# Kernel tuning notes

Measured on AMD Instinct MI355X. Metric: run time of the kernel, lower is better.

The kernel has to match this reference:

```python
import jax, jax.numpy as jnp
import numpy as np

NODELEN = 10


def setup_inputs() -> dict:
    key = jax.random.key(0)
    ks = jax.random.split(key, 16)
    N, DEG = 200000, 32
    IN, H1, H2, EMB = 2 * NODELEN, 15, 10, 5
    features = jax.random.normal(ks[0], (N, NODELEN), dtype=jnp.float32)
    adj = jax.random.randint(ks[1], (N, DEG), 0, N, dtype=jnp.int32)
    s = 0.1
    inp = {
        'features': features,
        'adj': adj,
        'We1': jax.random.normal(ks[2], (H1, IN), dtype=jnp.float32) * s,
        'be1': jnp.zeros((H1,), dtype=jnp.float32),
        'We2': jax.random.normal(ks[3], (H2, H1), dtype=jnp.float32) * s,
        'be2': jnp.zeros((H2,), dtype=jnp.float32),
        'We3': jax.random.normal(ks[4], (EMB, H2), dtype=jnp.float32) * s,
        'be3': jnp.zeros((EMB,), dtype=jnp.float32),
        'Wd1': jax.random.normal(ks[5], (H2, EMB), dtype=jnp.float32) * s,
        'bd1': jnp.zeros((H2,), dtype=jnp.float32),
        'Wd2': jax.random.normal(ks[6], (H1, H2), dtype=jnp.float32) * s,
        'bd2': jnp.zeros((H1,), dtype=jnp.float32),
        'Wd3': jax.random.normal(ks[7], (IN, H1), dtype=jnp.float32) * s,
        'bd3': jnp.zeros((IN,), dtype=jnp.float32),
    }
    return inp


def _autoencoder(x, We1, be1, We2, be2, We3, be3, Wd1, bd1, Wd2, bd2, Wd3, bd3):
    # torch nn.Linear: y = x @ W.T + b ; dropout is identity in eval
    h = jax.nn.relu(x @ We1.T + be1)
    h = jax.nn.relu(h @ We2.T + be2)
    encoded = h @ We3.T + be3
    h = jax.nn.relu(encoded @ Wd1.T + bd1)
    h = jax.nn.relu(h @ Wd2.T + bd2)
    decoded = h @ Wd3.T + bd3
    return encoded, decoded


def reference(features, adj, We1, be1, We2, be2, We3, be3,
              Wd1, bd1, Wd2, bd2, Wd3, bd3):
    # depth-2 recursive neighbor aggregation (aggregate_neighbors):
    # hop 1: mean of raw neighbor features, element 0 zeroed
    h1 = jnp.mean(features[adj], axis=1)          # [N, deg, F] -> [N, F]
    h1 = h1.at[:, 0].set(0.0)
    # hop 2: mean of hop-1 features of neighbors, element 0 zeroed
    agg = jnp.mean(h1[adj], axis=1)
    agg = agg.at[:, 0].set(0.0)
    # generate_embedding: concat(self, aggregated), zero positions 0 and NODELEN
    emb = jnp.concatenate([features, agg], axis=1)
    emb = emb.at[:, 0].set(0.0).at[:, NODELEN].set(0.0)
    encoded, decoded = _autoencoder(emb, We1, be1, We2, be2, We3, be3,
                                    Wd1, bd1, Wd2, bd2, Wd3, bd3)
    return encoded, decoded, emb
```

## Files before the change

kernel.cpp:

```cpp
#include <hip/hip_runtime.h>

#define NODELEN 10
#define DEG 32
#define NPB 64


#if defined(__has_builtin)
#if __has_builtin(__builtin_amdgcn_cvt_pk_f32_fp8)
#define USE_HW_FP8_DECODE 1
#endif
#endif

typedef float floatx2 __attribute__((ext_vector_type(2)));

__device__ __forceinline__ float fp8_to_f32_sw(unsigned b) {
    unsigned s = (b & 0x80u) << 24;
    unsigned e = (b >> 3) & 0xFu;
    unsigned m = b & 0x7u;
    float fn = __uint_as_float(s | ((e + 120u) << 23) | (m << 20));
    float fs = __uint_as_float(s | __float_as_uint((float)m * 0.001953125f));
    return e ? fn : fs;
}

__device__ __forceinline__ void dacc(float& a, float& b, unsigned w, int hi) {
#if defined(USE_HW_FP8_DECODE)
    floatx2 f = hi ? __builtin_amdgcn_cvt_pk_f32_fp8(w, true)
                   : __builtin_amdgcn_cvt_pk_f32_fp8(w, false);
    a += f.x; b += f.y;
#else
    unsigned p = hi ? (w >> 16) : w;
    a += fp8_to_f32_sw(p & 0xFFu);
    b += fp8_to_f32_sw((p >> 8) & 0xFFu);
#endif
}

__device__ __forceinline__ unsigned fp8_encode(float f) {
    unsigned u = __float_as_uint(f);
    unsigned s = u >> 31;
    float a = fabsf(f);
    if (a < 0.015625f) {
        int mi = __float2int_rn(a * 512.0f);
        return (s << 7) | (unsigned)mi;
    }
    int e = (int)((u >> 23) & 0xFFu) - 127;
    unsigned mant = u & 0x7FFFFFu;
    unsigned r = mant + 0x7FFFFu + ((mant >> 20) & 1u);
    mant = r >> 20;
    if (mant == 8u) { mant = 0u; e += 1; }
    return (s << 7) | ((unsigned)(e + 7) << 3) | mant;
}

__device__ __forceinline__ int4 pack_row_fp8(const float* v) {
    unsigned b[NODELEN];
#pragma unroll
    for (int k = 0; k < NODELEN; ++k) b[k] = fp8_encode(v[k]);
    int4 p;
    p.x = (int)(b[0] | (b[1] << 8) | (b[2] << 16) | (b[3] << 24));
    p.y = (int)(b[4] | (b[5] << 8) | (b[6] << 16) | (b[7] << 24));
    p.z = (int)(b[8] | (b[9] << 8));
    p.w = 0;
    return p;
}

__device__ __forceinline__ void row_acc(float* s, int4 p) {
    unsigned w0 = (unsigned)p.x, w1 = (unsigned)p.y, w2 = (unsigned)p.z;
    dacc(s[0], s[1], w0, 0);
    dacc(s[2], s[3], w0, 1);
    dacc(s[4], s[5], w1, 0);
    dacc(s[6], s[7], w1, 1);
    dacc(s[8], s[9], w2, 0);
}

__global__ __launch_bounds__(256) void prep_kernel(
    const float* __restrict__ features,
    int4*        __restrict__ f8feat,
    int N)
{
    int i = blockIdx.x * blockDim.x + threadIdx.x;
    if (i >= N) return;
    const float2* r = (const float2*)(features + (size_t)i * NODELEN);
    float2 a0 = r[0], a1 = r[1], a2 = r[2], a3 = r[3], a4 = r[4];
    float v[NODELEN] = {a0.x, a0.y, a1.x, a1.y, a2.x, a2.y, a3.x, a3.y, a4.x, a4.y};
    f8feat[i] = pack_row_fp8(v);
}

__global__ __launch_bounds__(256) void hop1_kernel(
    const int4* __restrict__ f8feat,
    const int*  __restrict__ adj,
    int4*       __restrict__ f8h1,
    int N)
{
    int t = blockIdx.x * blockDim.x + threadIdx.x;
    int i = t >> 2, sub = t & 3;
    if (i >= N) return;

    const int4* arow = (const int4*)(adj + (size_t)i * DEG + sub * 8);
    int4 n0 = arow[0], n1 = arow[1];

    float s[NODELEN];
#pragma unroll
    for (int k = 0; k < NODELEN; ++k) s[k] = 0.0f;
    row_acc(s, f8feat[n0.x]);
    row_acc(s, f8feat[n0.y]);
    row_acc(s, f8feat[n0.z]);
    row_acc(s, f8feat[n0.w]);
    row_acc(s, f8feat[n1.x]);
    row_acc(s, f8feat[n1.y]);
    row_acc(s, f8feat[n1.z]);
    row_acc(s, f8feat[n1.w]);

#pragma unroll
    for (int k = 0; k < NODELEN; ++k) {
        s[k] += __shfl_xor(s[k], 1);
        s[k] += __shfl_xor(s[k], 2);
    }

    if (sub == 0) {
        const float inv = 1.0f / (float)DEG;
        float h[NODELEN];
        h[0] = 0.0f;
#pragma unroll
        for (int k = 1; k < NODELEN; ++k) h[k] = s[k] * inv;
        f8h1[i] = pack_row_fp8(h);
    }
}

__global__ __launch_bounds__(256) void hop2_mlp_kernel(
    const float* __restrict__ features,
    const int*   __restrict__ adj,
    const int4*  __restrict__ f8h1,
    const float* __restrict__ We1, const float* __restrict__ be1,
    const float* __restrict__ We2, const float* __restrict__ be2,
    const float* __restrict__ We3, const float* __restrict__ be3,
    const float* __restrict__ Wd1, const float* __restrict__ bd1,
    const float* __restrict__ Wd2, const float* __restrict__ bd2,
    const float* __restrict__ Wd3, const float* __restrict__ bd3,
    float* __restrict__ out_enc,
    float* __restrict__ out_dec,
    float* __restrict__ out_emb,
    int N)
{
    __shared__ float  s_agg[NPB][11];
    __shared__ float4 s_feat4[NPB * 10 / 4];
    __shared__ float4 s_enc4[NPB * 5 / 4];
    __shared__ float4 s_dec4[NPB * 20 / 4];
    __shared__ float4 s_emb4[NPB * 20 / 4];

    const int tid  = threadIdx.x;
    const int base = blockIdx.x * NPB;
    const int nl   = tid >> 2, sub = tid & 3;
    const int i    = base + nl;
    const bool full = (base + NPB <= N);

    if (full) {
        const float4* gf = (const float4*)(features + (size_t)base * NODELEN);
        if (tid < NPB * 10 / 4) s_feat4[tid] = gf[tid];
    } else {
        int cnt = (N - base) * NODELEN;
        for (int k = tid; k < cnt; k += 256)
            ((float*)s_feat4)[k] = features[(size_t)base * NODELEN + k];
    }

    float s[NODELEN];
#pragma unroll
    for (int k = 0; k < NODELEN; ++k) s[k] = 0.0f;
    if (i < N) {
        const int4* arow = (const int4*)(adj + (size_t)i * DEG + sub * 8);
        int4 n0 = arow[0], n1 = arow[1];
        row_acc(s, f8h1[n0.x]);
        row_acc(s, f8h1[n0.y]);
        row_acc(s, f8h1[n0.z]);
        row_acc(s, f8h1[n0.w]);
        row_acc(s, f8h1[n1.x]);
        row_acc(s, f8h1[n1.y]);
        row_acc(s, f8h1[n1.z]);
        row_acc(s, f8h1[n1.w]);
    }
#pragma unroll
    for (int k = 0; k < NODELEN; ++k) {
        s[k] += __shfl_xor(s[k], 1);
        s[k] += __shfl_xor(s[k], 2);
    }
    if (sub == 0 && i < N) {
#pragma unroll
        for (int k = 0; k < NODELEN; ++k) s_agg[nl][k] = s[k];
    }
    __syncthreads();

    if (tid < NPB) {
        int node = base + tid;
        if (node < N) {
            const float inv = 1.0f / (float)DEG;
            const float* fr = (const float*)s_feat4 + tid * NODELEN;

            float emb[2 * NODELEN];
            emb[0] = 0.0f;
#pragma unroll
            for (int k = 1; k < NODELEN; ++k) emb[k] = fr[k];
            emb[NODELEN] = 0.0f;
#pragma unroll
            for (int k = 1; k < NODELEN; ++k) emb[NODELEN + k] = s_agg[tid][k] * inv;

            float t1[15];
#pragma unroll
            for (int o = 0; o < 15; ++o) {
                float acc = be1[o];
#pragma unroll
                for (int k = 0; k < 20; ++k) acc = fmaf(We1[o * 20 + k], emb[k], acc);
                t1[o] = fmaxf(acc, 0.0f);
            }
            float t2[10];
#pragma unroll
            for (int o = 0; o < 10; ++o) {
                float acc = be2[o];
#pragma unroll
                for (int k = 0; k < 15; ++k) acc = fmaf(We2[o * 15 + k], t1[k], acc);
                t2[o] = fmaxf(acc, 0.0f);
            }
            float enc[5];
#pragma unroll
            for (int o = 0; o < 5; ++o) {
                float acc = be3[o];
#pragma unroll
                for (int k = 0; k < 10; ++k) acc = fmaf(We3[o * 10 + k], t2[k], acc);
                enc[o] = acc;
            }
            float t3[10];
#pragma unroll
            for (int o = 0; o < 10; ++o) {
                float acc = bd1[o];
#pragma unroll
                for (int k = 0; k < 5; ++k) acc = fmaf(Wd1[o * 5 + k], enc[k], acc);
                t3[o] = fmaxf(acc, 0.0f);
            }
            float t4[15];
#pragma unroll
            for (int o = 0; o < 15; ++o) {
                float acc = bd2[o];
#pragma unroll
                for (int k = 0; k < 10; ++k) acc = fmaf(Wd2[o * 10 + k], t3[k], acc);
                t4[o] = fmaxf(acc, 0.0f);
            }
            float dec[20];
#pragma unroll
            for (int o = 0; o < 20; ++o) {
                float acc = bd3[o];
#pragma unroll
                for (int k = 0; k < 15; ++k) acc = fmaf(Wd3[o * 15 + k], t4[k], acc);
                dec[o] = acc;
            }

            float* se = (float*)s_enc4;
#pragma unroll
            for (int k = 0; k < 5; ++k) se[tid * 5 + k] = enc[k];
            float* sd = (float*)s_dec4;
#pragma unroll
            for (int k = 0; k < 20; ++k) sd[tid * 20 + k] = dec[k];
            float* sm = (float*)s_emb4;
#pragma unroll
            for (int k = 0; k < 20; ++k) sm[tid * 20 + k] = emb[k];
        }
    }
    __syncthreads();

    if (full) {
        float4* gd = (float4*)(out_dec + (size_t)base * 20);
#pragma unroll
        for (int k = tid; k < NPB * 20 / 4; k += 256) gd[k] = s_dec4[k];
        float4* gm = (float4*)(out_emb + (size_t)base * 20);
#pragma unroll
        for (int k = tid; k < NPB * 20 / 4; k += 256) gm[k] = s_emb4[k];
        float4* ge = (float4*)(out_enc + (size_t)base * 5);
        if (tid < NPB * 5 / 4) ge[tid] = s_enc4[tid];
    } else {
        int cnt = N - base;
        for (int k = tid; k < cnt * 20; k += 256)
            out_dec[(size_t)base * 20 + k] = ((float*)s_dec4)[k];
        for (int k = tid; k < cnt * 20; k += 256)
            out_emb[(size_t)base * 20 + k] = ((float*)s_emb4)[k];
        for (int k = tid; k < cnt * 5; k += 256)
            out_enc[(size_t)base * 5 + k] = ((float*)s_enc4)[k];
    }
}

extern "C" void kernel_launch(void* const* d_in, const int* in_sizes, int n_in,
                              void* d_out, int out_size, void* d_ws, size_t ws_size,
                              hipStream_t stream)
{
    const float* features = (const float*)d_in[0];
    const int*   adj      = (const int*)  d_in[1];
    const float* We1 = (const float*)d_in[2];  const float* be1 = (const float*)d_in[3];
    const float* We2 = (const float*)d_in[4];  const float* be2 = (const float*)d_in[5];
    const float* We3 = (const float*)d_in[6];  const float* be3 = (const float*)d_in[7];
    const float* Wd1 = (const float*)d_in[8];  const float* bd1 = (const float*)d_in[9];
    const float* Wd2 = (const float*)d_in[10]; const float* bd2 = (const float*)d_in[11];
    const float* Wd3 = (const float*)d_in[12]; const float* bd3 = (const float*)d_in[13];

    const int N = in_sizes[0] / NODELEN;

    int4* f8feat = (int4*)d_ws;
    int4* f8h1   = (int4*)((char*)d_ws + (size_t)N * 16);

    float* out     = (float*)d_out;
    float* out_enc = out;
    float* out_dec = out + (size_t)N * 5;
    float* out_emb = out + (size_t)N * 25;

    const int threads = 256;

    hipLaunchKernelGGL(prep_kernel, dim3((N + 255) / 256), dim3(threads), 0, stream,
                       features, f8feat, N);
    hipLaunchKernelGGL(hop1_kernel, dim3((4 * N + 255) / 256), dim3(threads), 0, stream,
                       f8feat, adj, f8h1, N);
    hipLaunchKernelGGL(hop2_mlp_kernel, dim3((N + NPB - 1) / NPB), dim3(threads), 0, stream,
                       features, adj, f8h1,
                       We1, be1, We2, be2, We3, be3,
                       Wd1, bd1, Wd2, bd2, Wd3, bd3,
                       out_enc, out_dec, out_emb, N);
}
```

Baseline: 181.8 us.

## Stage neighbor gathers through async global-to-LDS loads and drop tail guards

Both gather kernels now issue the eight neighbor-row fetches as asynchronous global-to-LDS loads into a per-wave staging buffer, wait once on vmcnt, then read the rows back from LDS to accumulate. The aim is to keep many gathers in flight without using vector registers and to cut latency stalls. The hop2 kernel also removes its partial-block bounds checks and reuses one shared buffer for staging and outputs. Dropping the guards assumes N is a multiple of 64 (it is, at 200000), so any other N would read and write out of bounds. The staging buffer also raises LDS usage, which may lower occupancy.

```diff
diff --git a/kernel.cpp b/kernel.cpp
--- a/kernel.cpp
+++ b/kernel.cpp
@@ -9,9 +9,22 @@
 #if __has_builtin(__builtin_amdgcn_cvt_pk_f32_fp8)
 #define USE_HW_FP8_DECODE 1
 #endif
+#if __has_builtin(__builtin_amdgcn_global_load_lds)
+#define HAS_ASYNC_LDS 1
+#endif
 #endif
 
 typedef float floatx2 __attribute__((ext_vector_type(2)));
+
+__device__ __forceinline__ void async_load16(const void* g, void* lds) {
+#if defined(HAS_ASYNC_LDS)
+    __builtin_amdgcn_global_load_lds(
+        (const __attribute__((address_space(1))) void*)g,
+        (__attribute__((address_space(3))) void*)lds,
+        16, 0, 0);
+#endif
+}
+#define WAIT_VM0() __builtin_amdgcn_s_waitcnt(0x0F70)
 
 __device__ __forceinline__ float fp8_to_f32_sw(unsigned b) {
     unsigned s = (b & 0x80u) << 24;
@@ -69,6 +82,12 @@
     dacc(s[4], s[5], w1, 0);
     dacc(s[6], s[7], w1, 1);
     dacc(s[8], s[9], w2, 0);
+}
+
+__device__ __forceinline__ void gather8_acc(float* s, const int4* __restrict__ tab,
+                                            const int* idxs) {
+#pragma unroll
+    for (int r = 0; r < 8; ++r) row_acc(s, tab[idxs[r]]);
 }
 
 __global__ __launch_bounds__(256) void prep_kernel(
@@ -90,24 +109,33 @@
     int4*       __restrict__ f8h1,
     int N)
 {
-    int t = blockIdx.x * blockDim.x + threadIdx.x;
-    int i = t >> 2, sub = t & 3;
+    __shared__ int4 s_stage[4 * 8 * 64];
+
+    const int tid = threadIdx.x;
+    const int t = blockIdx.x * blockDim.x + tid;
+    const int i = t >> 2, sub = t & 3;
     if (i >= N) return;
+    const int wid = tid >> 6, lane = tid & 63;
 
     const int4* arow = (const int4*)(adj + (size_t)i * DEG + sub * 8);
     int4 n0 = arow[0], n1 = arow[1];
+    int idxs[8] = {n0.x, n0.y, n0.z, n0.w, n1.x, n1.y, n1.z, n1.w};
 
     float s[NODELEN];
 #pragma unroll
     for (int k = 0; k < NODELEN; ++k) s[k] = 0.0f;
-    row_acc(s, f8feat[n0.x]);
-    row_acc(s, f8feat[n0.y]);
-    row_acc(s, f8feat[n0.z]);
-    row_acc(s, f8feat[n0.w]);
-    row_acc(s, f8feat[n1.x]);
-    row_acc(s, f8feat[n1.y]);
-    row_acc(s, f8feat[n1.z]);
-    row_acc(s, f8feat[n1.w]);
+
+#if defined(HAS_ASYNC_LDS)
+#pragma unroll
+    for (int r = 0; r < 8; ++r)
+        async_load16(f8feat + idxs[r], s_stage + (wid * 8 + r) * 64);
+    WAIT_VM0();
+#pragma unroll
+    for (int r = 0; r < 8; ++r)
+        row_acc(s, s_stage[(wid * 8 + r) * 64 + lane]);
+#else
+    gather8_acc(s, f8feat, idxs);
+#endif
 
 #pragma unroll
     for (int k = 0; k < NODELEN; ++k) {
@@ -140,146 +168,139 @@
     float* __restrict__ out_emb,
     int N)
 {
+    __shared__ char   s_mem[32768];
     __shared__ float  s_agg[NPB][11];
     __shared__ float4 s_feat4[NPB * 10 / 4];
-    __shared__ float4 s_enc4[NPB * 5 / 4];
-    __shared__ float4 s_dec4[NPB * 20 / 4];
-    __shared__ float4 s_emb4[NPB * 20 / 4];
+
+    int4*  s_stage = (int4*)s_mem;
+    float* s_enc   = (float*)s_mem;
+    float* s_dec   = (float*)(s_mem + 1280);
+    float* s_emb   = (float*)(s_mem + 6400);
 
     const int tid  = threadIdx.x;
     const int base = blockIdx.x * NPB;
     const int nl   = tid >> 2, sub = tid & 3;
     const int i    = base + nl;
-    const bool full = (base + NPB <= N);
-
-    if (full) {
+    const int wid  = tid >> 6, lane = tid & 63;
+
+    {
         const float4* gf = (const float4*)(features + (size_t)base * NODELEN);
         if (tid < NPB * 10 / 4) s_feat4[tid] = gf[tid];
-    } else {
-        int cnt = (N - base) * NODELEN;
-        for (int k = tid; k < cnt; k += 256)
-            ((float*)s_feat4)[k] = features[(size_t)base * NODELEN + k];
-    }
+    }
+
+    const int4* arow = (const int4*)(adj + (size_t)i * DEG + sub * 8);
+    int4 n0 = arow[0], n1 = arow[1];
+    int idxs[8] = {n0.x, n0.y, n0.z, n0.w, n1.x, n1.y, n1.z, n1.w};
 
     float s[NODELEN];
 #pragma unroll
     for (int k = 0; k < NODELEN; ++k) s[k] = 0.0f;
-    if (i < N) {
-        const int4* arow = (const int4*)(adj + (size_t)i * DEG + sub * 8);
-        int4 n0 = arow[0], n1 = arow[1];
-        row_acc(s, f8h1[n0.x]);
-        row_acc(s, f8h1[n0.y]);
-        row_acc(s, f8h1[n0.z]);
-        row_acc(s, f8h1[n0.w]);
-        row_acc(s, f8h1[n1.x]);
-        row_acc(s, f8h1[n1.y]);
-        row_acc(s, f8h1[n1.z]);
-        row_acc(s, f8h1[n1.w]);
-    }
+
+#if defined(HAS_ASYNC_LDS)
+#pragma unroll
+    for (int r = 0; r < 8; ++r)
+        async_load16(f8h1 + idxs[r], s_stage + (wid * 8 + r) * 64);
+    WAIT_VM0();
+#pragma unroll
+    for (int r = 0; r < 8; ++r)
+        row_acc(s, s_stage[(wid * 8 + r) * 64 + lane]);
+#else
+    gather8_acc(s, f8h1, idxs);
+#endif
+
 #pragma unroll
     for (int k = 0; k < NODELEN; ++k) {
         s[k] += __shfl_xor(s[k], 1);
         s[k] += __shfl_xor(s[k], 2);
     }
-    if (sub == 0 && i < N) {
+    if (sub == 0) {
 #pragma unroll
         for (int k = 0; k < NODELEN; ++k) s_agg[nl][k] = s[k];
     }
     __syncthreads();
 
     if (tid < NPB) {
-        int node = base + tid;
-        if (node < N) {
-            const float inv = 1.0f / (float)DEG;
-            const float* fr = (const float*)s_feat4 + tid * NODELEN;
-
-            float emb[2 * NODELEN];
-            emb[0] = 0.0f;
-#pragma unroll
-            for (int k = 1; k < NODELEN; ++k) emb[k] = fr[k];
-            emb[NODELEN] = 0.0f;
-#pragma unroll
-            for (int k = 1; k < NODELEN; ++k) emb[NODELEN + k] = s_agg[tid][k] * inv;
-
-            float t1[15];
-#pragma unroll
-            for (int o = 0; o < 15; ++o) {
-                float acc = be1[o];
-#pragma unroll
-                for (int k = 0; k < 20; ++k) acc = fmaf(We1[o * 20 + k], emb[k], acc);
-                t1[o] = fmaxf(acc, 0.0f);
-            }
-            float t2[10];
-#pragma unroll
-            for (int o = 0; o < 10; ++o) {
-                float acc = be2[o];
-#pragma unroll
-                for (int k = 0; k < 15; ++k) acc = fmaf(We2[o * 15 + k], t1[k], acc);
-                t2[o] = fmaxf(acc, 0.0f);
-            }
-            float enc[5];
-#pragma unroll
-            for (int o = 0; o < 5; ++o) {
-                float acc = be3[o];
-#pragma unroll
-                for (int k = 0; k < 10; ++k) acc = fmaf(We3[o * 10 + k], t2[k], acc);
-                enc[o] = acc;
-            }
-            float t3[10];
-#pragma unroll
-            for (int o = 0; o < 10; ++o) {
-                float acc = bd1[o];
-#pragma unroll
-                for (int k = 0; k < 5; ++k) acc = fmaf(Wd1[o * 5 + k], enc[k], acc);
-                t3[o] = fmaxf(acc, 0.0f);
-            }
-            float t4[15];
-#pragma unroll
-            for (int o = 0; o < 15; ++o) {
-                float acc = bd2[o];
-#pragma unroll
-                for (int k = 0; k < 10; ++k) acc = fmaf(Wd2[o * 10 + k], t3[k], acc);
-                t4[o] = fmaxf(acc, 0.0f);
-            }
-            float dec[20];
-#pragma unroll
-            for (int o = 0; o < 20; ++o) {
-                float acc = bd3[o];
-#pragma unroll
-                for (int k = 0; k < 15; ++k) acc = fmaf(Wd3[o * 15 + k], t4[k], acc);
-                dec[o] = acc;
-            }
-
-            float* se = (float*)s_enc4;
-#pragma unroll
-            for (int k = 0; k < 5; ++k) se[tid * 5 + k] = enc[k];
-            float* sd = (float*)s_dec4;
-#pragma unroll
-            for (int k = 0; k < 20; ++k) sd[tid * 20 + k] = dec[k];
-            float* sm = (float*)s_emb4;
-#pragma unroll
-            for (int k = 0; k < 20; ++k) sm[tid * 20 + k] = emb[k];
-        }
+        const float inv = 1.0f / (float)DEG;
+        const float* fr = (const float*)s_feat4 + tid * NODELEN;
+
+        float emb[2 * NODELEN];
+        emb[0] = 0.0f;
+#pragma unroll
+        for (int k = 1; k < NODELEN; ++k) emb[k] = fr[k];
+        emb[NODELEN] = 0.0f;
+#pragma unroll
+        for (int k = 1; k < NODELEN; ++k) emb[NODELEN + k] = s_agg[tid][k] * inv;
+
+        float t1[15];
+#pragma unroll
+        for (int o = 0; o < 15; ++o) {
+            float acc = be1[o];
+#pragma unroll
+            for (int k = 0; k < 20; ++k) acc = fmaf(We1[o * 20 + k], emb[k], acc);
+            t1[o] = fmaxf(acc, 0.0f);
+        }
+        float t2[10];
+#pragma unroll
+        for (int o = 0; o < 10; ++o) {
+            float acc = be2[o];
+#pragma unroll
+            for (int k = 0; k < 15; ++k) acc = fmaf(We2[o * 15 + k], t1[k], acc);
+            t2[o] = fmaxf(acc, 0.0f);
+        }
+        float enc[5];
+#pragma unroll
+        for (int o = 0; o < 5; ++o) {
+            float acc = be3[o];
+#pragma unroll
+            for (int k = 0; k < 10; ++k) acc = fmaf(We3[o * 10 + k], t2[k], acc);
+            enc[o] = acc;
+        }
+        float t3[10];
+#pragma unroll
+        for (int o = 0; o < 10; ++o) {
+            float acc = bd1[o];
+#pragma unroll
+            for (int k = 0; k < 5; ++k) acc = fmaf(Wd1[o * 5 + k], enc[k], acc);
+            t3[o] = fmaxf(acc, 0.0f);
+        }
+        float t4[15];
+#pragma unroll
+        for (int o = 0; o < 15; ++o) {
+            float acc = bd2[o];
+#pragma unroll
+            for (int k = 0; k < 10; ++k) acc = fmaf(Wd2[o * 10 + k], t3[k], acc);
+            t4[o] = fmaxf(acc, 0.0f);
+        }
+        float dec[20];
+#pragma unroll
+        for (int o = 0; o < 20; ++o) {
+            float acc = bd3[o];
+#pragma unroll
+            for (int k = 0; k < 15; ++k) acc = fmaf(Wd3[o * 15 + k], t4[k], acc);
+            dec[o] = acc;
+        }
+
+#pragma unroll
+        for (int k = 0; k < 5; ++k)  s_enc[tid * 5 + k]  = enc[k];
+#pragma unroll
+        for (int k = 0; k < 20; ++k) s_dec[tid * 20 + k] = dec[k];
+#pragma unroll
+        for (int k = 0; k < 20; ++k) s_emb[tid * 20 + k] = emb[k];
     }
     __syncthreads();
 
-    if (full) {
+    {
         float4* gd = (float4*)(out_dec + (size_t)base * 20);
-#pragma unroll
-        for (int k = tid; k < NPB * 20 / 4; k += 256) gd[k] = s_dec4[k];
+        const float4* sd4 = (const float4*)s_dec;
+#pragma unroll
+        for (int k = tid; k < NPB * 20 / 4; k += 256) gd[k] = sd4[k];
         float4* gm = (float4*)(out_emb + (size_t)base * 20);
-#pragma unroll
-        for (int k = tid; k < NPB * 20 / 4; k += 256) gm[k] = s_emb4[k];
+        const float4* sm4 = (const float4*)s_emb;
+#pragma unroll
+        for (int k = tid; k < NPB * 20 / 4; k += 256) gm[k] = sm4[k];
         float4* ge = (float4*)(out_enc + (size_t)base * 5);
-        if (tid < NPB * 5 / 4) ge[tid] = s_enc4[tid];
-    } else {
-        int cnt = N - base;
-        for (int k = tid; k < cnt * 20; k += 256)
-            out_dec[(size_t)base * 20 + k] = ((float*)s_dec4)[k];
-        for (int k = tid; k < cnt * 20; k += 256)
-            out_emb[(size_t)base * 20 + k] = ((float*)s_emb4)[k];
-        for (int k = tid; k < cnt * 5; k += 256)
-            out_enc[(size_t)base * 5 + k] = ((float*)s_enc4)[k];
+        const float4* se4 = (const float4*)s_enc;
+        if (tid < NPB * 5 / 4) ge[tid] = se4[tid];
     }
 }
 
```

Measured after the change: 193.3 us. +6.3%, slower.
